# Optimization experiments

Measured on AMD Instinct MI355X. Metric: run time of the kernel, lower is better.

The kernel has to match this reference:

```python
import jax, jax.numpy as jnp
import numpy as np

LN_EPS = 1e-5

def setup_inputs() -> dict:
    key = jax.random.key(0)
    ks = jax.random.split(key, 8)
    B, N, C = 8, 16384, 256
    x = jax.random.normal(ks[0], (B, N, C), dtype=jnp.float32)
    time_decay = jax.random.normal(ks[1], (C,), dtype=jnp.float32) * 0.1
    s = 1.0 / np.sqrt(C)
    W_k = jax.random.normal(ks[2], (C, C), dtype=jnp.float32) * s
    W_v = jax.random.normal(ks[3], (C, C), dtype=jnp.float32) * s
    W_r = jax.random.normal(ks[4], (C, C), dtype=jnp.float32) * s
    W_o = jax.random.normal(ks[5], (C, C), dtype=jnp.float32) * s
    ln_w = jnp.ones((C,), dtype=jnp.float32)
    ln_b = jnp.zeros((C,), dtype=jnp.float32)
    return {"x": x, "time_decay": time_decay, "W_k": W_k, "W_v": W_v,
            "W_r": W_r, "W_o": W_o, "ln_w": ln_w, "ln_b": ln_b}

def _layernorm(x, w, b):
    mu = jnp.mean(x, axis=-1, keepdims=True)
    var = jnp.mean(jnp.square(x - mu), axis=-1, keepdims=True)
    return (x - mu) * jax.lax.rsqrt(var + LN_EPS) * w + b

def reference(x, time_decay, W_k, W_v, W_r, W_o, ln_w, ln_b):
    # x: (B, N, C)
    xn = _layernorm(x, ln_w, ln_b)
    k = jnp.einsum('bnc,dc->bnd', xn, W_k)
    v = jnp.einsum('bnc,dc->bnd', xn, W_v)
    r = jax.nn.sigmoid(jnp.einsum('bnc,dc->bnd', xn, W_r))
    decay = jnp.exp(-jax.nn.relu(time_decay))  # (C,)

    def step(state, k_t):
        state = state * decay + k_t  # (B, C)
        return state, state

    k_tm = jnp.swapaxes(k, 0, 1)  # (N, B, C) time-major for scan
    init = jnp.zeros(k.shape[::2], dtype=x.dtype)  # (B, C)
    _, states = jax.lax.scan(step, init, k_tm)
    states = jnp.swapaxes(states, 0, 1)  # (B, N, C)
    y = r * (states + v)
    y = jnp.einsum('bnc,dc->bnd', y, W_o)
    return y
```

## Files before the change

kernel.cpp:

```cpp
#include <hip/hip_runtime.h>
#include <hip/hip_bf16.h>
#include <stdint.h>


typedef __attribute__((ext_vector_type(8))) short short8;
typedef __attribute__((ext_vector_type(4))) float f32x4;

static __device__ __forceinline__ unsigned short f2bf(float f) {
  __hip_bfloat16 h = __float2bfloat16(f);
  return *reinterpret_cast<unsigned short*>(&h);
}
static __device__ __forceinline__ float bf2f(unsigned short u) {
  unsigned int v = ((unsigned int)u) << 16;
  float f;
  __builtin_memcpy(&f, &v, 4);
  return f;
}

__global__ void ln_kernel(const float* __restrict__ x,
                          const float* __restrict__ w,
                          const float* __restrict__ b,
                          unsigned short* __restrict__ xn) {
  const int wv = threadIdx.x >> 6;
  const int ln = threadIdx.x & 63;
  const size_t row = (size_t)blockIdx.x * 4 + wv;
  const float4 v = reinterpret_cast<const float4*>(x)[row * 64 + ln];
  float s  = v.x + v.y + v.z + v.w;
  float sq = v.x * v.x + v.y * v.y + v.z * v.z + v.w * v.w;
#pragma unroll
  for (int off = 32; off; off >>= 1) {
    s  += __shfl_xor(s, off, 64);
    sq += __shfl_xor(sq, off, 64);
  }
  const float mu  = s * (1.0f / 256.0f);
  const float var = sq * (1.0f / 256.0f) - mu * mu;
  const float rs  = rsqrtf(var + 1e-5f);
  const float4 w4 = reinterpret_cast<const float4*>(w)[ln];
  const float4 b4 = reinterpret_cast<const float4*>(b)[ln];
  ushort4 o;
  o.x = f2bf((v.x - mu) * rs * w4.x + b4.x);
  o.y = f2bf((v.y - mu) * rs * w4.y + b4.y);
  o.z = f2bf((v.z - mu) * rs * w4.z + b4.z);
  o.w = f2bf((v.w - mu) * rs * w4.w + b4.w);
  reinterpret_cast<ushort4*>(xn)[row * 64 + ln] = o;
}

__global__ void cvt_weights(const float* __restrict__ Wk,
                            const float* __restrict__ Wv,
                            const float* __restrict__ Wr,
                            const float* __restrict__ Wo,
                            unsigned short* __restrict__ Wkvr,
                            unsigned short* __restrict__ Wob) {
  const int idx = blockIdx.x * 256 + threadIdx.x;
  if (idx < 768 * 256) {
    const int r = idx >> 8;
    const int c = idx & 255;
    const float* src = (r < 256) ? Wk : ((r < 512) ? Wv : Wr);
    Wkvr[idx] = f2bf(src[(r & 255) * 256 + c]);
  } else {
    const int j = idx - 768 * 256;
    Wob[j] = f2bf(Wo[j]);
  }
}

template <int EPI, int NY>
__global__ void gemm_bt(const unsigned short* __restrict__ A,
                        const unsigned short* __restrict__ Bt,
                        unsigned short* __restrict__ kbuf,
                        unsigned short* __restrict__ vbuf,
                        unsigned short* __restrict__ rbuf,
                        float* __restrict__ outf) {
  constexpr int K = 256;
  __shared__ unsigned short Als[128][64];
  __shared__ unsigned short Bls[128][64];

  const int tid = threadIdx.x;
  const int wv = tid >> 6;
  const int ln = tid & 63;
  const int bid = blockIdx.x;
  const int bm0 = (bid / NY) * 128;
  const int bn0 = (bid % NY) * 128;
  const int lq = ln >> 4;
  const int lm = ln & 15;

  f32x4 acc[4][4];
#pragma unroll
  for (int i = 0; i < 4; ++i)
#pragma unroll
    for (int j = 0; j < 4; ++j) acc[i][j] = (f32x4){0.f, 0.f, 0.f, 0.f};

  const int m0w = (wv >> 1) * 64;
  const int n0w = (wv & 1) * 64;

  const int srow = ln >> 3;
  const int schunk = (ln & 7) ^ srow;

  for (int kk0 = 0; kk0 < K; kk0 += 64) {
#pragma unroll
    for (int i = 0; i < 4; ++i) {
      const int rr = wv * 32 + i * 8;
      const unsigned short* gA = A + (size_t)(bm0 + rr + srow) * K + kk0 + schunk * 8;
      __builtin_amdgcn_global_load_lds(
          (const __attribute__((address_space(1))) void*)gA,
          (__attribute__((address_space(3))) void*)&Als[rr][0], 16, 0, 0);
      const unsigned short* gB = Bt + (size_t)(bn0 + rr + srow) * K + kk0 + schunk * 8;
      __builtin_amdgcn_global_load_lds(
          (const __attribute__((address_space(1))) void*)gB,
          (__attribute__((address_space(3))) void*)&Bls[rr][0], 16, 0, 0);
    }
    __syncthreads();
#pragma unroll
    for (int kk = 0; kk < 64; kk += 32) {
      short8 af[4], bfr[4];
      const int chunk = (kk >> 3) + lq;
#pragma unroll
      for (int t = 0; t < 4; ++t) {
        const int rowa = m0w + t * 16 + lm;
        af[t] = *reinterpret_cast<const short8*>(&Als[rowa][(chunk ^ (rowa & 7)) * 8]);
        const int rowb = n0w + t * 16 + lm;
        bfr[t] = *reinterpret_cast<const short8*>(&Bls[rowb][(chunk ^ (rowb & 7)) * 8]);
      }
#pragma unroll
      for (int mt = 0; mt < 4; ++mt)
#pragma unroll
        for (int nt = 0; nt < 4; ++nt)
          acc[mt][nt] = __builtin_amdgcn_mfma_f32_16x16x32_bf16(
              bfr[nt], af[mt], acc[mt][nt], 0, 0, 0);
    }
    __syncthreads();
  }

#pragma unroll
  for (int mt = 0; mt < 4; ++mt) {
    const int m_g = bm0 + m0w + mt * 16 + lm;
#pragma unroll
    for (int nt = 0; nt < 4; ++nt) {
      const int n_base = bn0 + n0w + nt * 16 + lq * 4;
      f32x4 a = acc[mt][nt];
      if (EPI == 0) {
        const int bufi = n_base >> 8;
        const int col = n_base & 255;
        unsigned short* dst = (bufi == 0) ? kbuf : ((bufi == 1) ? vbuf : rbuf);
        if (bufi == 2) {
#pragma unroll
          for (int r = 0; r < 4; ++r) a[r] = 1.0f / (1.0f + __expf(-a[r]));
        }
        ushort4 pk;
        pk.x = f2bf(a[0]); pk.y = f2bf(a[1]); pk.z = f2bf(a[2]); pk.w = f2bf(a[3]);
        *reinterpret_cast<ushort4*>(&dst[(size_t)m_g * 256 + col]) = pk;
      } else {
        float4 o = make_float4(a[0], a[1], a[2], a[3]);
        *reinterpret_cast<float4*>(&outf[(size_t)m_g * 256 + n_base]) = o;
      }
    }
  }
}

__global__ void scan_carry(const unsigned short* __restrict__ k,
                           const float* __restrict__ td,
                           float* __restrict__ carry) {
  const int lane32 = threadIdx.x & 31;
  const int sub = threadIdx.x >> 5;
  const int bch = blockIdx.x * 8 + sub;
  const int c0 = lane32 * 8;
  float d[8], s[8];
#pragma unroll
  for (int j = 0; j < 8; ++j) {
    d[j] = expf(-fmaxf(td[c0 + j], 0.0f));
    s[j] = 0.0f;
  }
  const unsigned short* kp = k + (size_t)bch * 64 * 256 + c0;
#pragma unroll 4
  for (int i = 0; i < 64; ++i) {
    short8 kv = *reinterpret_cast<const short8*>(kp + (size_t)i * 256);
#pragma unroll
    for (int j = 0; j < 8; ++j) s[j] = s[j] * d[j] + bf2f((unsigned short)kv[j]);
  }
  float4* cp = reinterpret_cast<float4*>(carry + (size_t)bch * 256 + c0);
  cp[0] = make_float4(s[0], s[1], s[2], s[3]);
  cp[1] = make_float4(s[4], s[5], s[6], s[7]);
}

__global__ void scan_chunks(float* __restrict__ carry,
                            const float* __restrict__ td) {
  const int b = blockIdx.x;
  const int c = threadIdx.x;
  const float dL = expf(-fmaxf(td[c], 0.0f) * 64.0f);
  float s = 0.0f;
  float* base = carry + (size_t)b * 256 * 256 + c;
  for (int j0 = 0; j0 < 256; j0 += 8) {
    float buf[8];
#pragma unroll
    for (int t = 0; t < 8; ++t) buf[t] = base[(size_t)(j0 + t) * 256];
#pragma unroll
    for (int t = 0; t < 8; ++t) {
      base[(size_t)(j0 + t) * 256] = s;
      s = dL * s + buf[t];
    }
  }
}

__global__ void scan_final(unsigned short* __restrict__ k,
                           const unsigned short* __restrict__ v,
                           const unsigned short* __restrict__ r,
                           const float* __restrict__ carryin,
                           const float* __restrict__ td) {
  const int lane32 = threadIdx.x & 31;
  const int sub = threadIdx.x >> 5;
  const int bch = blockIdx.x * 8 + sub;
  const int c0 = lane32 * 8;
  float d[8], s[8];
  const float4* ci = reinterpret_cast<const float4*>(carryin + (size_t)bch * 256 + c0);
  float4 c0v = ci[0], c1v = ci[1];
  s[0] = c0v.x; s[1] = c0v.y; s[2] = c0v.z; s[3] = c0v.w;
  s[4] = c1v.x; s[5] = c1v.y; s[6] = c1v.z; s[7] = c1v.w;
#pragma unroll
  for (int j = 0; j < 8; ++j) d[j] = expf(-fmaxf(td[c0 + j], 0.0f));
  const size_t base = (size_t)bch * 64 * 256 + c0;
#pragma unroll 2
  for (int i = 0; i < 64; ++i) {
    const size_t off = base + (size_t)i * 256;
    short8 kv = *reinterpret_cast<const short8*>(k + off);
    short8 vv = *reinterpret_cast<const short8*>(v + off);
    short8 rv = *reinterpret_cast<const short8*>(r + off);
    short8 y;
#pragma unroll
    for (int j = 0; j < 8; ++j) {
      s[j] = s[j] * d[j] + bf2f((unsigned short)kv[j]);
      const float yj = bf2f((unsigned short)rv[j]) * (s[j] + bf2f((unsigned short)vv[j]));
      y[j] = (short)f2bf(yj);
    }
    *reinterpret_cast<short8*>(k + off) = y;
  }
}

extern "C" void kernel_launch(void* const* d_in, const int* in_sizes, int n_in,
                              void* d_out, int out_size, void* d_ws, size_t ws_size,
                              hipStream_t stream) {
  const float* x   = (const float*)d_in[0];
  const float* td  = (const float*)d_in[1];
  const float* Wk  = (const float*)d_in[2];
  const float* Wv  = (const float*)d_in[3];
  const float* Wr  = (const float*)d_in[4];
  const float* Wo  = (const float*)d_in[5];
  const float* lnw = (const float*)d_in[6];
  const float* lnb = (const float*)d_in[7];
  float* out = (float*)d_out;

  const int Bsz = 8, C = 256;
  const size_t M = 131072;

  char* ws = (char*)d_ws;
  size_t off = 0;
  auto alloc = [&](size_t bytes) -> char* {
    char* p = ws + off;
    off += (bytes + 255) & ~(size_t)255;
    return p;
  };
  unsigned short* xn   = (unsigned short*)alloc(M * C * 2);
  unsigned short* kbuf = (unsigned short*)alloc(M * C * 2);
  unsigned short* vbuf = (unsigned short*)alloc(M * C * 2);
  unsigned short* rbuf = (unsigned short*)alloc(M * C * 2);
  unsigned short* Wkvr = (unsigned short*)alloc(768 * 256 * 2);
  unsigned short* Wob  = (unsigned short*)alloc(256 * 256 * 2);
  float* carry = (float*)alloc((size_t)Bsz * 256 * C * 4);
  (void)ws_size; (void)in_sizes; (void)n_in; (void)out_size;

  cvt_weights<<<dim3(1024), dim3(256), 0, stream>>>(Wk, Wv, Wr, Wo, Wkvr, Wob);
  ln_kernel<<<dim3((unsigned)(M / 4)), dim3(256), 0, stream>>>(x, lnw, lnb, xn);
  gemm_bt<0, 6><<<dim3(1024 * 6), dim3(256), 0, stream>>>(
      xn, Wkvr, kbuf, vbuf, rbuf, nullptr);
  scan_carry<<<dim3(256), dim3(256), 0, stream>>>(kbuf, td, carry);
  scan_chunks<<<dim3(Bsz), dim3(256), 0, stream>>>(carry, td);
  scan_final<<<dim3(256), dim3(256), 0, stream>>>(kbuf, vbuf, rbuf, carry, td);
  gemm_bt<1, 2><<<dim3(1024 * 2), dim3(256), 0, stream>>>(
      kbuf, Wob, nullptr, nullptr, nullptr, out);
}
```

Baseline: 440.3 us.

## Fuse scan into single decoupled-lookback kernel, merge LN with weight convert, XCD-aware GEMM tiling

Replaces the three-kernel chunked scan (carry, chunk prefix, final) with one kernel. Each block computes its local aggregate, publishes it with a flag, and walks back over predecessors using decoupled lookback to get its inclusive prefix. LayerNorm, weight conversion and flag reset are merged into one launch, and GEMM block indices are remapped so consecutive M tiles land on the same XCD for L2 reuse. This cuts launch count and the carry round trips, but relies on forward progress of predecessor blocks and adds spin-wait latency.

```diff
diff --git a/kernel.cpp b/kernel.cpp
--- a/kernel.cpp
+++ b/kernel.cpp
@@ -17,49 +17,55 @@
   return f;
 }
 
-__global__ void ln_kernel(const float* __restrict__ x,
-                          const float* __restrict__ w,
-                          const float* __restrict__ b,
-                          unsigned short* __restrict__ xn) {
-  const int wv = threadIdx.x >> 6;
-  const int ln = threadIdx.x & 63;
-  const size_t row = (size_t)blockIdx.x * 4 + wv;
-  const float4 v = reinterpret_cast<const float4*>(x)[row * 64 + ln];
-  float s  = v.x + v.y + v.z + v.w;
-  float sq = v.x * v.x + v.y * v.y + v.z * v.z + v.w * v.w;
-#pragma unroll
-  for (int off = 32; off; off >>= 1) {
-    s  += __shfl_xor(s, off, 64);
-    sq += __shfl_xor(sq, off, 64);
-  }
-  const float mu  = s * (1.0f / 256.0f);
-  const float var = sq * (1.0f / 256.0f) - mu * mu;
-  const float rs  = rsqrtf(var + 1e-5f);
-  const float4 w4 = reinterpret_cast<const float4*>(w)[ln];
-  const float4 b4 = reinterpret_cast<const float4*>(b)[ln];
-  ushort4 o;
-  o.x = f2bf((v.x - mu) * rs * w4.x + b4.x);
-  o.y = f2bf((v.y - mu) * rs * w4.y + b4.y);
-  o.z = f2bf((v.z - mu) * rs * w4.z + b4.z);
-  o.w = f2bf((v.w - mu) * rs * w4.w + b4.w);
-  reinterpret_cast<ushort4*>(xn)[row * 64 + ln] = o;
-}
-
-__global__ void cvt_weights(const float* __restrict__ Wk,
-                            const float* __restrict__ Wv,
-                            const float* __restrict__ Wr,
-                            const float* __restrict__ Wo,
-                            unsigned short* __restrict__ Wkvr,
-                            unsigned short* __restrict__ Wob) {
-  const int idx = blockIdx.x * 256 + threadIdx.x;
-  if (idx < 768 * 256) {
-    const int r = idx >> 8;
-    const int c = idx & 255;
-    const float* src = (r < 256) ? Wk : ((r < 512) ? Wv : Wr);
-    Wkvr[idx] = f2bf(src[(r & 255) * 256 + c]);
+__global__ void k1_fused(const float* __restrict__ x,
+                         const float* __restrict__ lnw,
+                         const float* __restrict__ lnb,
+                         const float* __restrict__ Wk,
+                         const float* __restrict__ Wv,
+                         const float* __restrict__ Wr,
+                         const float* __restrict__ Wo,
+                         unsigned short* __restrict__ xn,
+                         unsigned short* __restrict__ Wkvr,
+                         unsigned short* __restrict__ Wob,
+                         int* __restrict__ flags) {
+  const int bid = blockIdx.x;
+  if (bid < 32768) {
+    const int wv = threadIdx.x >> 6;
+    const int ln = threadIdx.x & 63;
+    const size_t row = (size_t)bid * 4 + wv;
+    const float4 v = reinterpret_cast<const float4*>(x)[row * 64 + ln];
+    float s  = v.x + v.y + v.z + v.w;
+    float sq = v.x * v.x + v.y * v.y + v.z * v.z + v.w * v.w;
+#pragma unroll
+    for (int off = 32; off; off >>= 1) {
+      s  += __shfl_xor(s, off, 64);
+      sq += __shfl_xor(sq, off, 64);
+    }
+    const float mu  = s * (1.0f / 256.0f);
+    const float var = sq * (1.0f / 256.0f) - mu * mu;
+    const float rs  = rsqrtf(var + 1e-5f);
+    const float4 w4 = reinterpret_cast<const float4*>(lnw)[ln];
+    const float4 b4 = reinterpret_cast<const float4*>(lnb)[ln];
+    ushort4 o;
+    o.x = f2bf((v.x - mu) * rs * w4.x + b4.x);
+    o.y = f2bf((v.y - mu) * rs * w4.y + b4.y);
+    o.z = f2bf((v.z - mu) * rs * w4.z + b4.z);
+    o.w = f2bf((v.w - mu) * rs * w4.w + b4.w);
+    reinterpret_cast<ushort4*>(xn)[row * 64 + ln] = o;
+  } else if (bid < 33792) {
+    const int idx = (bid - 32768) * 256 + threadIdx.x;
+    if (idx < 768 * 256) {
+      const int r = idx >> 8;
+      const int c = idx & 255;
+      const float* src = (r < 256) ? Wk : ((r < 512) ? Wv : Wr);
+      Wkvr[idx] = f2bf(src[(r & 255) * 256 + c]);
+    } else {
+      const int j = idx - 768 * 256;
+      Wob[j] = f2bf(Wo[j]);
+    }
   } else {
-    const int j = idx - 768 * 256;
-    Wob[j] = f2bf(Wo[j]);
+    flags[threadIdx.x] = 0;
+    flags[threadIdx.x + 256] = 0;
   }
 }
 
@@ -78,8 +84,10 @@
   const int wv = tid >> 6;
   const int ln = tid & 63;
   const int bid = blockIdx.x;
-  const int bm0 = (bid / NY) * 128;
-  const int bn0 = (bid % NY) * 128;
+  const int xcd = bid & 7;
+  const int j = bid >> 3;
+  const int bm0 = (xcd * 128 + j / NY) * 128;
+  const int bn0 = (j % NY) * 128;
   const int lq = ln >> 4;
   const int lm = ln & 15;
 
@@ -87,7 +95,7 @@
 #pragma unroll
   for (int i = 0; i < 4; ++i)
 #pragma unroll
-    for (int j = 0; j < 4; ++j) acc[i][j] = (f32x4){0.f, 0.f, 0.f, 0.f};
+    for (int jj = 0; jj < 4; ++jj) acc[i][jj] = (f32x4){0.f, 0.f, 0.f, 0.f};
 
   const int m0w = (wv >> 1) * 64;
   const int n0w = (wv & 1) * 64;
@@ -156,79 +164,120 @@
   }
 }
 
-__global__ void scan_carry(const unsigned short* __restrict__ k,
-                           const float* __restrict__ td,
-                           float* __restrict__ carry) {
-  const int lane32 = threadIdx.x & 31;
-  const int sub = threadIdx.x >> 5;
-  const int bch = blockIdx.x * 8 + sub;
-  const int c0 = lane32 * 8;
-  float d[8], s[8];
-#pragma unroll
-  for (int j = 0; j < 8; ++j) {
-    d[j] = expf(-fmaxf(td[c0 + j], 0.0f));
-    s[j] = 0.0f;
-  }
-  const unsigned short* kp = k + (size_t)bch * 64 * 256 + c0;
-#pragma unroll 4
-  for (int i = 0; i < 64; ++i) {
-    short8 kv = *reinterpret_cast<const short8*>(kp + (size_t)i * 256);
-#pragma unroll
-    for (int j = 0; j < 8; ++j) s[j] = s[j] * d[j] + bf2f((unsigned short)kv[j]);
-  }
-  float4* cp = reinterpret_cast<float4*>(carry + (size_t)bch * 256 + c0);
-  cp[0] = make_float4(s[0], s[1], s[2], s[3]);
-  cp[1] = make_float4(s[4], s[5], s[6], s[7]);
-}
-
-__global__ void scan_chunks(float* __restrict__ carry,
-                            const float* __restrict__ td) {
-  const int b = blockIdx.x;
-  const int c = threadIdx.x;
-  const float dL = expf(-fmaxf(td[c], 0.0f) * 64.0f);
-  float s = 0.0f;
-  float* base = carry + (size_t)b * 256 * 256 + c;
-  for (int j0 = 0; j0 < 256; j0 += 8) {
-    float buf[8];
-#pragma unroll
-    for (int t = 0; t < 8; ++t) buf[t] = base[(size_t)(j0 + t) * 256];
-#pragma unroll
-    for (int t = 0; t < 8; ++t) {
-      base[(size_t)(j0 + t) * 256] = s;
-      s = dL * s + buf[t];
-    }
-  }
-}
-
-__global__ void scan_final(unsigned short* __restrict__ k,
+__global__ void scan_fused(unsigned short* __restrict__ k,
                            const unsigned short* __restrict__ v,
                            const unsigned short* __restrict__ r,
-                           const float* __restrict__ carryin,
-                           const float* __restrict__ td) {
-  const int lane32 = threadIdx.x & 31;
-  const int sub = threadIdx.x >> 5;
-  const int bch = blockIdx.x * 8 + sub;
-  const int c0 = lane32 * 8;
-  float d[8], s[8];
-  const float4* ci = reinterpret_cast<const float4*>(carryin + (size_t)bch * 256 + c0);
-  float4 c0v = ci[0], c1v = ci[1];
-  s[0] = c0v.x; s[1] = c0v.y; s[2] = c0v.z; s[3] = c0v.w;
-  s[4] = c1v.x; s[5] = c1v.y; s[6] = c1v.z; s[7] = c1v.w;
-#pragma unroll
-  for (int j = 0; j < 8; ++j) d[j] = expf(-fmaxf(td[c0 + j], 0.0f));
-  const size_t base = (size_t)bch * 64 * 256 + c0;
+                           const float* __restrict__ td,
+                           float* __restrict__ carryA,
+                           float* __restrict__ prefixP,
+                           int* __restrict__ flags) {
+  __shared__ float lsP[8][256];
+  __shared__ float lsS[8][256];
+  __shared__ int fstat;
+
+  const int blk = blockIdx.x;
+  const int jb = blk & 63;
+  const int tid = threadIdx.x;
+  const int sub = tid >> 5;
+  const int lane = tid & 31;
+  const int c0 = lane * 8;
+
+  float d[8];
+#pragma unroll
+  for (int jj = 0; jj < 8; ++jj) d[jj] = __expf(-fmaxf(td[c0 + jj], 0.0f));
+
+  const size_t base = ((size_t)blk * 256 + sub * 32) * 256 + c0;
+  float s[8];
+#pragma unroll
+  for (int jj = 0; jj < 8; ++jj) s[jj] = 0.0f;
+#pragma unroll 4
+  for (int i = 0; i < 32; ++i) {
+    short8 kv = *reinterpret_cast<const short8*>(k + base + (size_t)i * 256);
+#pragma unroll
+    for (int jj = 0; jj < 8; ++jj) s[jj] = s[jj] * d[jj] + bf2f((unsigned short)kv[jj]);
+  }
+#pragma unroll
+  for (int jj = 0; jj < 8; ++jj) lsP[sub][c0 + jj] = s[jj];
+  __syncthreads();
+
+  const float dc  = __expf(-fmaxf(td[tid], 0.0f));
+  const float dB  = __expf(-fmaxf(td[tid], 0.0f) * 32.0f);
+  const float dS  = __expf(-fmaxf(td[tid], 0.0f) * 256.0f);
+  float a_blk = 0.0f;
+#pragma unroll
+  for (int s8 = 0; s8 < 8; ++s8) a_blk = dB * a_blk + lsP[s8][tid];
+
+  float s_in_blk;
+  if (jb == 0) {
+    prefixP[(size_t)blk * 256 + tid] = a_blk;
+    __threadfence();
+    __syncthreads();
+    if (tid == 0)
+      __hip_atomic_store(&flags[blk], 2, __ATOMIC_RELEASE, __HIP_MEMORY_SCOPE_AGENT);
+    s_in_blk = 0.0f;
+  } else {
+    carryA[(size_t)blk * 256 + tid] = a_blk;
+    __threadfence();
+    __syncthreads();
+    if (tid == 0)
+      __hip_atomic_store(&flags[blk], 1, __ATOMIC_RELEASE, __HIP_MEMORY_SCOPE_AGENT);
+    float acc = 0.0f, w = 1.0f;
+    int pred = blk - 1;
+    for (;;) {
+      if (tid == 0) {
+        int f;
+        do {
+          f = __hip_atomic_load(&flags[pred], __ATOMIC_ACQUIRE, __HIP_MEMORY_SCOPE_AGENT);
+          if (f == 0) __builtin_amdgcn_s_sleep(8);
+        } while (f == 0);
+        fstat = f;
+      }
+      __syncthreads();
+      const int f = fstat;
+      __threadfence();
+      if (f == 2) {
+        acc += w * prefixP[(size_t)pred * 256 + tid];
+        break;
+      }
+      acc += w * carryA[(size_t)pred * 256 + tid];
+      w *= dS;
+      --pred;
+      __syncthreads();
+    }
+    s_in_blk = acc;
+    prefixP[(size_t)blk * 256 + tid] = dS * s_in_blk + a_blk;
+    __threadfence();
+    __syncthreads();
+    if (tid == 0)
+      __hip_atomic_store(&flags[blk], 2, __ATOMIC_RELEASE, __HIP_MEMORY_SCOPE_AGENT);
+  }
+
+  {
+    float cur = s_in_blk;
+#pragma unroll
+    for (int s8 = 0; s8 < 8; ++s8) {
+      lsS[s8][tid] = cur;
+      cur = dB * cur + lsP[s8][tid];
+    }
+  }
+  (void)dc;
+  __syncthreads();
+
+  float st[8];
+#pragma unroll
+  for (int jj = 0; jj < 8; ++jj) st[jj] = lsS[sub][c0 + jj];
 #pragma unroll 2
-  for (int i = 0; i < 64; ++i) {
+  for (int i = 0; i < 32; ++i) {
     const size_t off = base + (size_t)i * 256;
     short8 kv = *reinterpret_cast<const short8*>(k + off);
     short8 vv = *reinterpret_cast<const short8*>(v + off);
     short8 rv = *reinterpret_cast<const short8*>(r + off);
     short8 y;
 #pragma unroll
-    for (int j = 0; j < 8; ++j) {
-      s[j] = s[j] * d[j] + bf2f((unsigned short)kv[j]);
-      const float yj = bf2f((unsigned short)rv[j]) * (s[j] + bf2f((unsigned short)vv[j]));
-      y[j] = (short)f2bf(yj);
+    for (int jj = 0; jj < 8; ++jj) {
+      st[jj] = st[jj] * d[jj] + bf2f((unsigned short)kv[jj]);
+      const float yj = bf2f((unsigned short)rv[jj]) * (st[jj] + bf2f((unsigned short)vv[jj]));
+      y[jj] = (short)f2bf(yj);
     }
     *reinterpret_cast<short8*>(k + off) = y;
   }
@@ -247,8 +296,8 @@
   const float* lnb = (const float*)d_in[7];
   float* out = (float*)d_out;
 
-  const int Bsz = 8, C = 256;
   const size_t M = 131072;
+  const int C = 256;
 
   char* ws = (char*)d_ws;
   size_t off = 0;
@@ -263,16 +312,17 @@
   unsigned short* rbuf = (unsigned short*)alloc(M * C * 2);
   unsigned short* Wkvr = (unsigned short*)alloc(768 * 256 * 2);
   unsigned short* Wob  = (unsigned short*)alloc(256 * 256 * 2);
-  float* carry = (float*)alloc((size_t)Bsz * 256 * C * 4);
+  float* carryA  = (float*)alloc(512 * 256 * 4);
+  float* prefixP = (float*)alloc(512 * 256 * 4);
+  int*   flags   = (int*)alloc(512 * 4);
   (void)ws_size; (void)in_sizes; (void)n_in; (void)out_size;
 
-  cvt_weights<<<dim3(1024), dim3(256), 0, stream>>>(Wk, Wv, Wr, Wo, Wkvr, Wob);
-  ln_kernel<<<dim3((unsigned)(M / 4)), dim3(256), 0, stream>>>(x, lnw, lnb, xn);
-  gemm_bt<0, 6><<<dim3(1024 * 6), dim3(256), 0, stream>>>(
+  k1_fused<<<dim3(33793), dim3(256), 0, stream>>>(
+      x, lnw, lnb, Wk, Wv, Wr, Wo, xn, Wkvr, Wob, flags);
+  gemm_bt<0, 6><<<dim3(6144), dim3(256), 0, stream>>>(
       xn, Wkvr, kbuf, vbuf, rbuf, nullptr);
-  scan_carry<<<dim3(256), dim3(256), 0, stream>>>(kbuf, td, carry);
-  scan_chunks<<<dim3(Bsz), dim3(256), 0, stream>>>(carry, td);
-  scan_final<<<dim3(256), dim3(256), 0, stream>>>(kbuf, vbuf, rbuf, carry, td);
-  gemm_bt<1, 2><<<dim3(1024 * 2), dim3(256), 0, stream>>>(
+  scan_fused<<<dim3(512), dim3(256), 0, stream>>>(
+      kbuf, vbuf, rbuf, td, carryA, prefixP, flags);
+  gemm_bt<1, 2><<<dim3(2048), dim3(256), 0, stream>>>(
       kbuf, Wob, nullptr, nullptr, nullptr, out);
 }
```

New measurement: 1.059 ms. 2.41x slower.
